# Kernel optimization log

Hardware: AMD Instinct MI355X
Metric: run time of the kernel (lower is better)

The kernel has to match this reference:

```python
import jax, jax.numpy as jnp
import numpy as np

B, T, E, U, H = 1024, 200, 64, 64, 4  # batch, hist_len, embed, num_units, head_num
NEG = -2.0**32 + 1  # padding value from the TF code
EPS = 1e-9


def setup_inputs() -> dict:
    key = jax.random.key(0)
    k1, k2, k3, k4 = jax.random.split(key, 4)
    input_info = jax.random.normal(k1, (B, T, E), dtype=jnp.float32)
    keys_length = jax.random.randint(k2, (B, 1), 1, T + 1)  # valid lengths in [1, T]
    W = jax.random.truncated_normal(k3, -2.0, 2.0, (E, 3 * U), dtype=jnp.float32) * 0.05
    W_output = jax.random.truncated_normal(k4, -2.0, 2.0, (U, U), dtype=jnp.float32) * 0.05
    gamma = jnp.ones((U,), dtype=jnp.float32)
    beta = jnp.zeros((U,), dtype=jnp.float32)
    return {"input_info": input_info, "keys_length": keys_length,
            "W": W, "W_output": W_output, "gamma": gamma, "beta": beta}


def reference(input_info, keys_length, W, W_output, gamma, beta):
    b, t, e = input_info.shape
    u = W_output.shape[0]
    dh = u // H  # per-head dim; TF scales by sqrt of this (post-split dim)
    qkv = input_info @ W                     # [B,T,3U]
    q, k, v = jnp.split(qkv, 3, axis=-1)     # each [B,T,U]
    q = q.reshape(b, t, H, dh)
    k = k.reshape(b, t, H, dh)
    v = v.reshape(b, t, H, dh)
    scores = jnp.einsum('bqhd,bkhd->bhqk', q, k) / jnp.sqrt(jnp.float32(dh))
    mask = jnp.arange(t)[None, :] < keys_length          # [B,T] key mask
    scores = jnp.where(mask[:, None, None, :], scores, jnp.float32(NEG))
    align = jax.nn.softmax(scores, axis=-1)              # [B,H,T,T]
    out = jnp.einsum('bhqk,bkhd->bqhd', align, v).reshape(b, t, u)
    out = out @ W_output                                 # output projection
    out = out + input_info                               # residual (dropout off at inference)
    mean = out.mean(axis=-1, keepdims=True)
    var = jnp.mean((out - mean) ** 2, axis=-1, keepdims=True)
    out = (out - mean) / jnp.sqrt(var + EPS) * gamma + beta  # layernorm
    return out
```

## Files before the change

### kernel.cpp

```cpp
#include <hip/hip_runtime.h>

#define B_  1024
#define T_  200
#define E_  64
#define U_  64
#define H_  4

typedef float f32x4   __attribute__((ext_vector_type(4)));
typedef float f32x16  __attribute__((ext_vector_type(16)));
typedef short bf16x8  __attribute__((ext_vector_type(8)));

static __device__ __forceinline__ unsigned short f2bf(float x) {
  unsigned u = __float_as_uint(x);
  u += 0x7FFFu + ((u >> 16) & 1u);
  return (unsigned short)(u >> 16);
}
static __device__ __forceinline__ float bf2f(unsigned short u) {
  return __uint_as_float(((unsigned)u) << 16);
}
static __device__ __forceinline__ float ldf(const void* p, long i, bool bf) {
  return bf ? bf2f(reinterpret_cast<const unsigned short*>(p)[i])
            : reinterpret_cast<const float*>(p)[i];
}

__global__ __launch_bounds__(512, 4)
void mha_mfma(const void* __restrict__ input,
              const void* __restrict__ keys_length,
              const void* __restrict__ W,
              const void* __restrict__ Wo,
              const void* __restrict__ gamma,
              const void* __restrict__ beta,
              float* __restrict__ out) {
  __shared__ __align__(16) short sQ[256 * 16];
  __shared__ __align__(16) short sK[256 * 16];
  __shared__ __align__(16) short sVt[16 * 264];
  __shared__ __align__(16) short sWt[48 * 72];
  __shared__ __align__(16) short sWoT[64 * 72];
  __shared__ __align__(16) short sP[8 * 32 * 40];
  __shared__ __align__(16) float sL[8 * 32];
  __shared__ float sGB[128];

  const int b    = blockIdx.x;
  const int tid  = threadIdx.x;
  const int wave = tid >> 6, lane = tid & 63;
  const int lane15 = lane & 15, quad = lane >> 4;
  const int lane31 = lane & 31, h5   = lane >> 5;

  const bool bf = (reinterpret_cast<const unsigned*>(gamma)[0] != 0x3F800000u);

  const unsigned* klu = reinterpret_cast<const unsigned*>(keys_length);
  const unsigned probe = klu[1];
  int len;
  if (probe == 0u)        len = (int)klu[2 * b];
  else if (probe <= 200u) len = (int)klu[b];
  else                    len = (int)__uint_as_float(klu[b]);
  len = len < 1 ? 1 : (len > T_ ? T_ : len);
  const int ntiles = (len + 31) >> 5;

  for (int i = tid; i < 64 * 64; i += 512) {
    int c = i & 63, r = i >> 6;
    sWoT[c * 72 + r] = (short)f2bf(ldf(Wo, (long)r * 64 + c, bf));
  }
  if (tid < 128) sGB[tid] = (tid < 64) ? ldf(gamma, tid, bf) : ldf(beta, tid - 64, bf);

  f32x16 oA, oB;
#pragma unroll
  for (int i = 0; i < 16; ++i) { oA[i] = 0.f; oB[i] = 0.f; }

  const int m32 = wave;
  short* myP = &sP[wave * (32 * 40)];
  const float* inpf = (const float*)input;

  for (int h = 0; h < H_; ++h) {
    for (int i = tid; i < 48 * 64; i += 512) {
      int jj = i % 48, e = i / 48;
      int col = (jj >> 4) * 64 + h * 16 + (jj & 15);
      sWt[jj * 72 + e] = (short)f2bf(ldf(W, (long)e * 192 + col, bf));
    }
    __syncthreads();

#pragma unroll
    for (int mi = 0; mi < 2; ++mi) {
      const int m16 = wave * 2 + mi;
      if (m16 < 14) {
        int tg = m16 * 16 + lane15; if (tg > 199) tg = 199;
        float af[2][8];
        if (!bf) {
          const float* rp = inpf + ((size_t)b * T_ + tg) * E_;
#pragma unroll
          for (int kh = 0; kh < 2; ++kh) {
            float4 u = *(const float4*)(rp + kh * 32 + quad * 8);
            float4 v = *(const float4*)(rp + kh * 32 + quad * 8 + 4);
            af[kh][0] = u.x; af[kh][1] = u.y; af[kh][2] = u.z; af[kh][3] = u.w;
            af[kh][4] = v.x; af[kh][5] = v.y; af[kh][6] = v.z; af[kh][7] = v.w;
          }
        } else {
#pragma unroll
          for (int kh = 0; kh < 2; ++kh)
#pragma unroll
            for (int j = 0; j < 8; ++j)
              af[kh][j] = ldf(input, ((long)b * T_ + tg) * E_ + kh * 32 + quad * 8 + j, true);
        }
        bf16x8 a0, a1;
#pragma unroll
        for (int j = 0; j < 8; ++j) { a0[j] = (short)f2bf(af[0][j]); a1[j] = (short)f2bf(af[1][j]); }
#pragma unroll
        for (int nn = 0; nn < 3; ++nn) {
          bf16x8 b0 = *(const bf16x8*)&sWt[(nn * 16 + lane15) * 72 + quad * 8];
          bf16x8 b1 = *(const bf16x8*)&sWt[(nn * 16 + lane15) * 72 + 32 + quad * 8];
          f32x4 acc; acc[0] = 0.f; acc[1] = 0.f; acc[2] = 0.f; acc[3] = 0.f;
          acc = __builtin_amdgcn_mfma_f32_16x16x32_bf16(a0, b0, acc, 0, 0, 0);
          acc = __builtin_amdgcn_mfma_f32_16x16x32_bf16(a1, b1, acc, 0, 0, 0);
          const int tr = m16 * 16 + quad * 4;
          if (nn == 0) {
#pragma unroll
            for (int r = 0; r < 4; ++r) sQ[(tr + r) * 16 + lane15] = (short)f2bf(acc[r] * 0.25f);
          } else if (nn == 1) {
#pragma unroll
            for (int r = 0; r < 4; ++r) sK[(tr + r) * 16 + lane15] = (short)f2bf(acc[r]);
          } else {
#pragma unroll
            for (int r = 0; r < 4; ++r) sVt[lane15 * 264 + tr + r] = (short)f2bf(acc[r]);
          }
        }
      }
    }
    __syncthreads();

    if (m32 < 7) {
      bf16x8 qa = *(const bf16x8*)&sQ[(m32 * 32 + lane31) * 16 + h5 * 8];
      f32x4 O0, O1;
#pragma unroll
      for (int r = 0; r < 4; ++r) { O0[r] = 0.f; O1[r] = 0.f; }
      float lv[16];
#pragma unroll
      for (int i = 0; i < 16; ++i) lv[i] = 0.f;

      for (int kt = 0; kt < ntiles; ++kt) {
        bf16x8 kb = *(const bf16x8*)&sK[(kt * 32 + lane31) * 16 + h5 * 8];
        f32x16 s;
#pragma unroll
        for (int i = 0; i < 16; ++i) s[i] = 0.f;
        s = __builtin_amdgcn_mfma_f32_32x32x16_bf16(qa, kb, s, 0, 0, 0);
        const int tk = kt * 32 + lane31;
        const float pm = (tk < len) ? 1.0f : 0.0f;
#pragma unroll
        for (int i = 0; i < 16; ++i) {
          float p = pm * __expf(s[i]);
          lv[i] += p;
          myP[((i & 3) + 8 * (i >> 2) + 4 * h5) * 40 + lane31] = (short)f2bf(p);
        }
        bf16x8 vf = *(const bf16x8*)&sVt[lane15 * 264 + kt * 32 + quad * 8];
        bf16x8 p0 = *(const bf16x8*)&myP[lane15 * 40 + quad * 8];
        bf16x8 p1 = *(const bf16x8*)&myP[(16 + lane15) * 40 + quad * 8];
        O0 = __builtin_amdgcn_mfma_f32_16x16x32_bf16(p0, vf, O0, 0, 0, 0);
        O1 = __builtin_amdgcn_mfma_f32_16x16x32_bf16(p1, vf, O1, 0, 0, 0);
      }
#pragma unroll
      for (int off = 1; off < 32; off <<= 1)
#pragma unroll
        for (int i = 0; i < 16; ++i) lv[i] += __shfl_xor(lv[i], off);
      if (lane31 == 0) {
#pragma unroll
        for (int i = 0; i < 16; ++i)
          sL[wave * 32 + (i & 3) + 8 * (i >> 2) + 4 * h5] = lv[i];
      }
      float l0[4], l1[4];
      *(float4*)l0 = *(const float4*)&sL[wave * 32 + quad * 4];
      *(float4*)l1 = *(const float4*)&sL[wave * 32 + 16 + quad * 4];
#pragma unroll
      for (int r = 0; r < 4; ++r) {
        myP[(quad * 4 + r) * 40 + lane15]      = (short)f2bf(O0[r] / l0[r]);
        myP[(16 + quad * 4 + r) * 40 + lane15] = (short)f2bf(O1[r] / l1[r]);
      }
      bf16x8 oa = *(const bf16x8*)&myP[lane31 * 40 + h5 * 8];
      bf16x8 w0 = *(const bf16x8*)&sWoT[lane31 * 72 + h * 16 + h5 * 8];
      bf16x8 w1 = *(const bf16x8*)&sWoT[(32 + lane31) * 72 + h * 16 + h5 * 8];
      oA = __builtin_amdgcn_mfma_f32_32x32x16_bf16(oa, w0, oA, 0, 0, 0);
      oB = __builtin_amdgcn_mfma_f32_32x32x16_bf16(oa, w1, oB, 0, 0, 0);
    }
  }

  if (m32 < 7) {
    const float g0 = sGB[lane31], g1 = sGB[32 + lane31];
    const float be0 = sGB[64 + lane31], be1 = sGB[96 + lane31];
#pragma unroll
    for (int i = 0; i < 16; ++i) {
      const int t = m32 * 32 + (i & 3) + 8 * (i >> 2) + 4 * h5;
      const bool valid = t < 200;
      const size_t base = ((size_t)b * T_ + t) * E_;
      float x0 = oA[i], x1 = oB[i];
      if (valid) {
        if (!bf) { x0 += inpf[base + lane31]; x1 += inpf[base + 32 + lane31]; }
        else     { x0 += ldf(input, base + lane31, true); x1 += ldf(input, base + 32 + lane31, true); }
      }
      float sx = x0 + x1, sxx = x0 * x0 + x1 * x1;
#pragma unroll
      for (int off = 1; off < 32; off <<= 1) {
        sx  += __shfl_xor(sx, off);
        sxx += __shfl_xor(sxx, off);
      }
      const float mean = sx * (1.0f / 64.0f);
      float var = sxx * (1.0f / 64.0f) - mean * mean;
      var = var < 0.f ? 0.f : var;
      const float inv = rsqrtf(var + 1e-9f);
      if (valid) {
        out[base + lane31]      = (x0 - mean) * inv * g0 + be0;
        out[base + 32 + lane31] = (x1 - mean) * inv * g1 + be1;
      }
    }
  }
}

static const void* pick_by_size(void* const* d_in, const int* in_sizes, int n_in,
                                int want, int which, const void* fallback) {
  int seen = 0;
  for (int i = 0; i < n_in; ++i) {
    if (in_sizes[i] == want) {
      if (seen == which) return d_in[i];
      ++seen;
    }
  }
  return fallback;
}

extern "C" void kernel_launch(void* const* d_in, const int* in_sizes, int n_in,
                              void* d_out, int out_size, void* d_ws, size_t ws_size,
                              hipStream_t stream) {
  const void* input  = pick_by_size(d_in, in_sizes, n_in, B_ * T_ * E_, 0, d_in[0]);
  const void* klen   = pick_by_size(d_in, in_sizes, n_in, B_,           0, d_in[1]);
  const void* W      = pick_by_size(d_in, in_sizes, n_in, E_ * 3 * U_,  0, d_in[2]);
  const void* Wo     = pick_by_size(d_in, in_sizes, n_in, U_ * U_,      0, d_in[3]);
  const void* gamma  = pick_by_size(d_in, in_sizes, n_in, U_,           0, d_in[4]);
  const void* beta   = pick_by_size(d_in, in_sizes, n_in, U_,           1, d_in[5]);
  float* o           = (float*)d_out;
  (void)out_size; (void)d_ws; (void)ws_size;
  mha_mfma<<<dim3(B_), dim3(512), 0, stream>>>(input, klen, W, Wo, gamma, beta, o);
}
```

Measured before the change: 212.8 us.

## Keep softmax probabilities in registers via permlane swap and skip padded K/V projection

Computes S^T (K as the A operand) so each lane owns one query column. The probabilities are packed to bf16 with v_cvt_pk_bf16_f32 and rearranged with permlane32_swap, then fed straight into the PV MFMA. This replaces the per-wave LDS round trip for P and the cross-lane row-sum shuffles. Q is pre-scaled by log2e/4 so exp2 can be used, and the QKV projection is split into per-matrix jobs so K/V tiles beyond the valid length are not computed. LDS indices are XOR-swizzled. In exchange, the PV MFMA now zero-pads half of its V operand, and normalization happens after a bf16 round trip of O.

```diff
diff --git a/kernel.cpp b/kernel.cpp
--- a/kernel.cpp
+++ b/kernel.cpp
@@ -9,12 +9,8 @@
 typedef float f32x4   __attribute__((ext_vector_type(4)));
 typedef float f32x16  __attribute__((ext_vector_type(16)));
 typedef short bf16x8  __attribute__((ext_vector_type(8)));
-
-static __device__ __forceinline__ unsigned short f2bf(float x) {
-  unsigned u = __float_as_uint(x);
-  u += 0x7FFFu + ((u >> 16) & 1u);
-  return (unsigned short)(u >> 16);
-}
+typedef unsigned uint2v __attribute__((ext_vector_type(2)));
+
 static __device__ __forceinline__ float bf2f(unsigned short u) {
   return __uint_as_float(((unsigned)u) << 16);
 }
@@ -22,6 +18,21 @@
   return bf ? bf2f(reinterpret_cast<const unsigned short*>(p)[i])
             : reinterpret_cast<const float*>(p)[i];
 }
+static __device__ __forceinline__ unsigned pkbf2(float lo, float hi) {
+  unsigned r;
+  asm("v_cvt_pk_bf16_f32 %0, %1, %2" : "=v"(r) : "v"(lo), "v"(hi));
+  return r;
+}
+static __device__ __forceinline__ void swap32(unsigned& a, unsigned& b) {
+#if defined(__has_builtin) && __has_builtin(__builtin_amdgcn_permlane32_swap)
+  uint2v r = __builtin_amdgcn_permlane32_swap(a, b, false, false);
+  a = r[0]; b = r[1];
+#else
+  asm volatile("v_permlane32_swap_b32 %0, %1" : "+v"(a), "+v"(b));
+#endif
+}
+
+#define QK_IDX(t, c) ((((t) << 4) + (c)) ^ ((((t) >> 2) & 1) << 3))
 
 __global__ __launch_bounds__(512, 4)
 void mha_mfma(const void* __restrict__ input,
@@ -31,13 +42,12 @@
               const void* __restrict__ gamma,
               const void* __restrict__ beta,
               float* __restrict__ out) {
-  __shared__ __align__(16) short sQ[256 * 16];
-  __shared__ __align__(16) short sK[256 * 16];
-  __shared__ __align__(16) short sVt[16 * 264];
+  __shared__ __align__(16) short sQ[224 * 16];
+  __shared__ __align__(16) short sK[224 * 16];
+  __shared__ __align__(16) short sVt[16 * 232];
   __shared__ __align__(16) short sWt[48 * 72];
   __shared__ __align__(16) short sWoT[64 * 72];
-  __shared__ __align__(16) short sP[8 * 32 * 40];
-  __shared__ __align__(16) float sL[8 * 32];
+  __shared__ __align__(16) short sO[7 * 32 * 16];
   __shared__ float sGB[128];
 
   const int b    = blockIdx.x;
@@ -56,10 +66,12 @@
   else                    len = (int)__uint_as_float(klu[b]);
   len = len < 1 ? 1 : (len > T_ ? T_ : len);
   const int ntiles = (len + 31) >> 5;
+  const int kvt16  = ntiles * 2;
+  const int njobs  = 14 + 2 * kvt16;
 
   for (int i = tid; i < 64 * 64; i += 512) {
     int c = i & 63, r = i >> 6;
-    sWoT[c * 72 + r] = (short)f2bf(ldf(Wo, (long)r * 64 + c, bf));
+    sWoT[c * 72 + r] = (short)pkbf2(ldf(Wo, (long)r * 64 + c, bf), 0.f);
   }
   if (tid < 128) sGB[tid] = (tid < 64) ? ldf(gamma, tid, bf) : ldf(beta, tid - 64, bf);
 
@@ -68,112 +80,143 @@
   for (int i = 0; i < 16; ++i) { oA[i] = 0.f; oB[i] = 0.f; }
 
   const int m32 = wave;
-  short* myP = &sP[wave * (32 * 40)];
   const float* inpf = (const float*)input;
 
   for (int h = 0; h < H_; ++h) {
     for (int i = tid; i < 48 * 64; i += 512) {
       int jj = i % 48, e = i / 48;
       int col = (jj >> 4) * 64 + h * 16 + (jj & 15);
-      sWt[jj * 72 + e] = (short)f2bf(ldf(W, (long)e * 192 + col, bf));
+      sWt[jj * 72 + e] = (short)pkbf2(ldf(W, (long)e * 192 + col, bf), 0.f);
     }
     __syncthreads();
 
-#pragma unroll
-    for (int mi = 0; mi < 2; ++mi) {
-      const int m16 = wave * 2 + mi;
-      if (m16 < 14) {
-        int tg = m16 * 16 + lane15; if (tg > 199) tg = 199;
-        float af[2][8];
-        if (!bf) {
-          const float* rp = inpf + ((size_t)b * T_ + tg) * E_;
-#pragma unroll
-          for (int kh = 0; kh < 2; ++kh) {
-            float4 u = *(const float4*)(rp + kh * 32 + quad * 8);
-            float4 v = *(const float4*)(rp + kh * 32 + quad * 8 + 4);
-            af[kh][0] = u.x; af[kh][1] = u.y; af[kh][2] = u.z; af[kh][3] = u.w;
-            af[kh][4] = v.x; af[kh][5] = v.y; af[kh][6] = v.z; af[kh][7] = v.w;
-          }
+    for (int job = wave; job < njobs; job += 8) {
+      int nn, m16;
+      if (job < 14)              { nn = 0; m16 = job; }
+      else if (job < 14 + kvt16) { nn = 1; m16 = job - 14; }
+      else                       { nn = 2; m16 = job - 14 - kvt16; }
+      int tg = m16 * 16 + lane15; if (tg > 199) tg = 199;
+      bf16x8 a0, a1;
+      unsigned* au0 = reinterpret_cast<unsigned*>(&a0);
+      unsigned* au1 = reinterpret_cast<unsigned*>(&a1);
+      if (!bf) {
+        const float* rp = inpf + ((size_t)b * T_ + tg) * E_ + quad * 8;
+        float4 u0 = *(const float4*)(rp);
+        float4 v0 = *(const float4*)(rp + 4);
+        float4 u1 = *(const float4*)(rp + 32);
+        float4 v1 = *(const float4*)(rp + 36);
+        au0[0] = pkbf2(u0.x, u0.y); au0[1] = pkbf2(u0.z, u0.w);
+        au0[2] = pkbf2(v0.x, v0.y); au0[3] = pkbf2(v0.z, v0.w);
+        au1[0] = pkbf2(u1.x, u1.y); au1[1] = pkbf2(u1.z, u1.w);
+        au1[2] = pkbf2(v1.x, v1.y); au1[3] = pkbf2(v1.z, v1.w);
+      } else {
+        float af[16];
+#pragma unroll
+        for (int kh = 0; kh < 2; ++kh)
+#pragma unroll
+          for (int j = 0; j < 8; ++j)
+            af[kh * 8 + j] = ldf(input, ((long)b * T_ + tg) * E_ + kh * 32 + quad * 8 + j, true);
+#pragma unroll
+        for (int j = 0; j < 4; ++j) au0[j] = pkbf2(af[2 * j], af[2 * j + 1]);
+#pragma unroll
+        for (int j = 0; j < 4; ++j) au1[j] = pkbf2(af[8 + 2 * j], af[8 + 2 * j + 1]);
+      }
+      bf16x8 b0 = *(const bf16x8*)&sWt[(nn * 16 + lane15) * 72 + quad * 8];
+      bf16x8 b1 = *(const bf16x8*)&sWt[(nn * 16 + lane15) * 72 + 32 + quad * 8];
+      f32x4 acc; acc[0] = 0.f; acc[1] = 0.f; acc[2] = 0.f; acc[3] = 0.f;
+      acc = __builtin_amdgcn_mfma_f32_16x16x32_bf16(a0, b0, acc, 0, 0, 0);
+      acc = __builtin_amdgcn_mfma_f32_16x16x32_bf16(a1, b1, acc, 0, 0, 0);
+      const int tr = m16 * 16 + quad * 4;
+      if (nn == 0) {
+        const float qs = 0.36067376f;
+        unsigned w01 = pkbf2(acc[0] * qs, acc[1] * qs);
+        unsigned w23 = pkbf2(acc[2] * qs, acc[3] * qs);
+        sQ[QK_IDX(tr + 0, lane15)] = (short)w01;
+        sQ[QK_IDX(tr + 1, lane15)] = (short)(w01 >> 16);
+        sQ[QK_IDX(tr + 2, lane15)] = (short)w23;
+        sQ[QK_IDX(tr + 3, lane15)] = (short)(w23 >> 16);
+      } else if (nn == 1) {
+        unsigned w01 = pkbf2(acc[0], acc[1]);
+        unsigned w23 = pkbf2(acc[2], acc[3]);
+        sK[QK_IDX(tr + 0, lane15)] = (short)w01;
+        sK[QK_IDX(tr + 1, lane15)] = (short)(w01 >> 16);
+        sK[QK_IDX(tr + 2, lane15)] = (short)w23;
+        sK[QK_IDX(tr + 3, lane15)] = (short)(w23 >> 16);
+      } else {
+        unsigned w01 = pkbf2(acc[0], acc[1]);
+        unsigned w23 = pkbf2(acc[2], acc[3]);
+        unsigned* vp = reinterpret_cast<unsigned*>(&sVt[lane15 * 232 + tr]);
+        vp[0] = w01; vp[1] = w23;
+      }
+    }
+    __syncthreads();
+
+    if (m32 < 7) {
+      bf16x8 qa = *(const bf16x8*)&sQ[QK_IDX(m32 * 32 + lane31, h5 * 8)];
+      f32x16 Oacc;
+#pragma unroll
+      for (int i = 0; i < 16; ++i) Oacc[i] = 0.f;
+      float lacc = 0.f;
+
+      for (int kt = 0; kt < ntiles; ++kt) {
+        bf16x8 kb = *(const bf16x8*)&sK[QK_IDX(kt * 32 + lane31, h5 * 8)];
+        f32x16 s;
+#pragma unroll
+        for (int i = 0; i < 16; ++i) s[i] = 0.f;
+        s = __builtin_amdgcn_mfma_f32_32x32x16_bf16(kb, qa, s, 0, 0, 0);
+        float p[16];
+        if (kt * 32 + 32 <= len) {
+#pragma unroll
+          for (int i = 0; i < 16; ++i) { p[i] = exp2f(s[i]); lacc += p[i]; }
         } else {
 #pragma unroll
-          for (int kh = 0; kh < 2; ++kh)
-#pragma unroll
-            for (int j = 0; j < 8; ++j)
-              af[kh][j] = ldf(input, ((long)b * T_ + tg) * E_ + kh * 32 + quad * 8 + j, true);
-        }
-        bf16x8 a0, a1;
-#pragma unroll
-        for (int j = 0; j < 8; ++j) { a0[j] = (short)f2bf(af[0][j]); a1[j] = (short)f2bf(af[1][j]); }
-#pragma unroll
-        for (int nn = 0; nn < 3; ++nn) {
-          bf16x8 b0 = *(const bf16x8*)&sWt[(nn * 16 + lane15) * 72 + quad * 8];
-          bf16x8 b1 = *(const bf16x8*)&sWt[(nn * 16 + lane15) * 72 + 32 + quad * 8];
-          f32x4 acc; acc[0] = 0.f; acc[1] = 0.f; acc[2] = 0.f; acc[3] = 0.f;
-          acc = __builtin_amdgcn_mfma_f32_16x16x32_bf16(a0, b0, acc, 0, 0, 0);
-          acc = __builtin_amdgcn_mfma_f32_16x16x32_bf16(a1, b1, acc, 0, 0, 0);
-          const int tr = m16 * 16 + quad * 4;
-          if (nn == 0) {
-#pragma unroll
-            for (int r = 0; r < 4; ++r) sQ[(tr + r) * 16 + lane15] = (short)f2bf(acc[r] * 0.25f);
-          } else if (nn == 1) {
-#pragma unroll
-            for (int r = 0; r < 4; ++r) sK[(tr + r) * 16 + lane15] = (short)f2bf(acc[r]);
-          } else {
-#pragma unroll
-            for (int r = 0; r < 4; ++r) sVt[lane15 * 264 + tr + r] = (short)f2bf(acc[r]);
+          for (int i = 0; i < 16; ++i) {
+            const int tk = kt * 32 + (i & 3) + 8 * (i >> 2) + 4 * h5;
+            const float e = exp2f(s[i]);
+            p[i] = (tk < len) ? e : 0.f;
+            lacc += p[i];
           }
         }
-      }
-    }
-    __syncthreads();
-
-    if (m32 < 7) {
-      bf16x8 qa = *(const bf16x8*)&sQ[(m32 * 32 + lane31) * 16 + h5 * 8];
-      f32x4 O0, O1;
-#pragma unroll
-      for (int r = 0; r < 4; ++r) { O0[r] = 0.f; O1[r] = 0.f; }
-      float lv[16];
-#pragma unroll
-      for (int i = 0; i < 16; ++i) lv[i] = 0.f;
-
-      for (int kt = 0; kt < ntiles; ++kt) {
-        bf16x8 kb = *(const bf16x8*)&sK[(kt * 32 + lane31) * 16 + h5 * 8];
-        f32x16 s;
-#pragma unroll
-        for (int i = 0; i < 16; ++i) s[i] = 0.f;
-        s = __builtin_amdgcn_mfma_f32_32x32x16_bf16(qa, kb, s, 0, 0, 0);
-        const int tk = kt * 32 + lane31;
-        const float pm = (tk < len) ? 1.0f : 0.0f;
-#pragma unroll
-        for (int i = 0; i < 16; ++i) {
-          float p = pm * __expf(s[i]);
-          lv[i] += p;
-          myP[((i & 3) + 8 * (i >> 2) + 4 * h5) * 40 + lane31] = (short)f2bf(p);
+#pragma unroll
+        for (int ks = 0; ks < 2; ++ks) {
+          unsigned c0 = pkbf2(p[8 * ks + 0], p[8 * ks + 1]);
+          unsigned c1 = pkbf2(p[8 * ks + 2], p[8 * ks + 3]);
+          unsigned c2 = pkbf2(p[8 * ks + 4], p[8 * ks + 5]);
+          unsigned c3 = pkbf2(p[8 * ks + 6], p[8 * ks + 7]);
+          swap32(c0, c2);
+          swap32(c1, c3);
+          bf16x8 pa;
+          unsigned* pw = reinterpret_cast<unsigned*>(&pa);
+          pw[0] = c0; pw[1] = c1; pw[2] = c2; pw[3] = c3;
+          bf16x8 vb;
+#pragma unroll
+          for (int z = 0; z < 8; ++z) vb[z] = 0;
+          if (lane31 < 16)
+            vb = *(const bf16x8*)&sVt[lane31 * 232 + kt * 32 + ks * 16 + h5 * 8];
+          Oacc = __builtin_amdgcn_mfma_f32_32x32x16_bf16(pa, vb, Oacc, 0, 0, 0);
         }
-        bf16x8 vf = *(const bf16x8*)&sVt[lane15 * 264 + kt * 32 + quad * 8];
-        bf16x8 p0 = *(const bf16x8*)&myP[lane15 * 40 + quad * 8];
-        bf16x8 p1 = *(const bf16x8*)&myP[(16 + lane15) * 40 + quad * 8];
-        O0 = __builtin_amdgcn_mfma_f32_16x16x32_bf16(p0, vf, O0, 0, 0, 0);
-        O1 = __builtin_amdgcn_mfma_f32_16x16x32_bf16(p1, vf, O1, 0, 0, 0);
-      }
-#pragma unroll
-      for (int off = 1; off < 32; off <<= 1)
-#pragma unroll
-        for (int i = 0; i < 16; ++i) lv[i] += __shfl_xor(lv[i], off);
-      if (lane31 == 0) {
-#pragma unroll
-        for (int i = 0; i < 16; ++i)
-          sL[wave * 32 + (i & 3) + 8 * (i >> 2) + 4 * h5] = lv[i];
-      }
-      float l0[4], l1[4];
-      *(float4*)l0 = *(const float4*)&sL[wave * 32 + quad * 4];
-      *(float4*)l1 = *(const float4*)&sL[wave * 32 + 16 + quad * 4];
-#pragma unroll
-      for (int r = 0; r < 4; ++r) {
-        myP[(quad * 4 + r) * 40 + lane15]      = (short)f2bf(O0[r] / l0[r]);
-        myP[(16 + quad * 4 + r) * 40 + lane15] = (short)f2bf(O1[r] / l1[r]);
-      }
-      bf16x8 oa = *(const bf16x8*)&myP[lane31 * 40 + h5 * 8];
+      }
+      lacc += __shfl_xor(lacc, 32);
+      const float rinv = 1.0f / lacc;
+#pragma unroll
+      for (int i = 0; i < 16; i += 2) {
+        const int r0 = (i & 3) + 8 * (i >> 2) + 4 * h5;
+        const unsigned w = pkbf2(Oacc[i], Oacc[i + 1]);
+        if (lane31 < 16) {
+          sO[(m32 << 9) + QK_IDX(r0,     lane31)] = (short)w;
+          sO[(m32 << 9) + QK_IDX(r0 + 1, lane31)] = (short)(w >> 16);
+        }
+      }
+      bf16x8 oraw = *(const bf16x8*)&sO[(m32 << 9) + QK_IDX(lane31, h5 * 8)];
+      const unsigned* op = reinterpret_cast<const unsigned*>(&oraw);
+      bf16x8 oa;
+      unsigned* np = reinterpret_cast<unsigned*>(&oa);
+#pragma unroll
+      for (int j = 0; j < 4; ++j) {
+        const float lo = __uint_as_float(op[j] << 16) * rinv;
+        const float hi = __uint_as_float(op[j] & 0xffff0000u) * rinv;
+        np[j] = pkbf2(lo, hi);
+      }
       bf16x8 w0 = *(const bf16x8*)&sWoT[lane31 * 72 + h * 16 + h5 * 8];
       bf16x8 w1 = *(const bf16x8*)&sWoT[(32 + lane31) * 72 + h * 16 + h5 * 8];
       oA = __builtin_amdgcn_mfma_f32_32x32x16_bf16(oa, w0, oA, 0, 0, 0);
```

Result: slower. 234.0 us (+9.9%).
